# Kernel optimization log

Hardware: AMD Instinct MI355X
Metric: run time of the kernel (lower is better)

Reference implementation:

```python
import jax, jax.numpy as jnp
import numpy as np

THR = 0.2
BORDER_RM = 2
TEMPERATURE = 0.1


def _border_valid(hc, wc, b):
    # True for grid cells at least b away from every border; flattened to [hc*wc]
    ih = jnp.arange(hc)
    iw = jnp.arange(wc)
    vh = (ih >= b) & (ih < hc - b)
    vw = (iw >= b) & (iw < wc - b)
    return (vh[:, None] & vw[None, :]).reshape(-1)


def setup_inputs() -> dict:
    key = jax.random.key(0)
    k0, k1 = jax.random.split(key)
    N, C = 4, 256
    h0c = w0c = h1c = w1c = 64  # 512/8 coarse grid
    feat_c0 = jax.random.normal(k0, (N, h0c * w0c, C), dtype=jnp.float32)
    feat_c1 = jax.random.normal(k1, (N, h1c * w1c, C), dtype=jnp.float32)
    return {"feat_c0": feat_c0, "feat_c1": feat_c1,
            "h0c": h0c, "w0c": w0c, "h1c": h1c, "w1c": w1c}


def reference(feat_c0, feat_c1, h0c, w0c, h1c, w1c):
    C = feat_c0.shape[-1]
    inv_sqrt_c = 1.0 / np.sqrt(C)
    f0 = feat_c0 * inv_sqrt_c
    f1 = feat_c1 * inv_sqrt_c
    # [N, L, S] similarity, dual softmax
    sim = jnp.einsum('nlc,nsc->nls', f0, f1) / TEMPERATURE
    conf = jax.nn.softmax(sim, axis=1) * jax.nn.softmax(sim, axis=2)
    # threshold + border suppression (eval path: mask_border)
    mask = conf > THR
    v0 = _border_valid(h0c, w0c, BORDER_RM)  # [L]
    v1 = _border_valid(h1c, w1c, BORDER_RM)  # [S]
    mask = mask & v0[None, :, None] & v1[None, None, :]
    # mutual top-1 (argmax along both rows and columns)
    mask = mask & (conf == conf.max(axis=2, keepdims=True)) \
                & (conf == conf.max(axis=1, keepdims=True))
    # per-row match: padded fixed-shape form of torch.where(mask_v)
    mask_v = mask.any(axis=2)                     # [N, L] bool: row i has a match
    j_ids = jnp.argmax(mask, axis=2)              # [N, L] matched column (0 if none)
    mconf = jnp.take_along_axis(conf, j_ids[..., None], axis=2)[..., 0]
    mconf = jnp.where(mask_v, mconf, 0.0)         # zero where no match (== m_bids filter)
    return conf, mask_v, j_ids.astype(jnp.int32), mconf
```

## Files before the change

kernel.cpp:

```cpp
#include <hip/hip_runtime.h>

#define L_DIM 4096
#define C_DIM 256
#define NB 4

typedef __bf16 bf16x8 __attribute__((ext_vector_type(8)));
typedef float f32x4 __attribute__((ext_vector_type(4)));

#define GLB __attribute__((address_space(1)))
#define AS3 __attribute__((address_space(3)))

__global__ void init_ws(float* __restrict__ rsum, float* __restrict__ csum,
                        unsigned int* __restrict__ colmax,
                        unsigned long long* __restrict__ rowpack) {
    int i = blockIdx.x * 256 + threadIdx.x;
    if (i < NB * L_DIM) { rsum[i] = 0.f; csum[i] = 0.f; colmax[i] = 0u; rowpack[i] = 0ull; }
}

__global__ __launch_bounds__(256) void conv_k(const float* __restrict__ in,
                                              __bf16* __restrict__ out) {
    int i = blockIdx.x * 256 + threadIdx.x;
    const float4* p = (const float4*)in + (size_t)i * 2;
    float4 a = p[0], b = p[1];
    bf16x8 v;
    v[0]=(__bf16)a.x; v[1]=(__bf16)a.y; v[2]=(__bf16)a.z; v[3]=(__bf16)a.w;
    v[4]=(__bf16)b.x; v[5]=(__bf16)b.y; v[6]=(__bf16)b.z; v[7]=(__bf16)b.w;
    *(bf16x8*)&out[(size_t)i * 8] = v;
}

__global__ void recip_k(float* __restrict__ rsum, float* __restrict__ csum) {
    int i = blockIdx.x * 256 + threadIdx.x;
    if (i < NB * L_DIM) { rsum[i] = 1.0f / rsum[i]; csum[i] = 1.0f / csum[i]; }
}

template<bool PRE, int MODE>
__global__ __launch_bounds__(256) void gemm_pass(
        const float* __restrict__ f0, const float* __restrict__ f1,
        const __bf16* __restrict__ a_bf, const __bf16* __restrict__ b_bf,
        float* __restrict__ E,
        float* __restrict__ rsum, float* __restrict__ csum,
        unsigned long long* __restrict__ rowpack, unsigned int* __restrict__ colmax) {
    const int n  = blockIdx.z;
    const int tl = blockIdx.y;
    const int ts = blockIdx.x;

    constexpr int LDST = PRE ? 64 : 72;
    __shared__ __bf16 Al[128 * LDST];
    __shared__ __bf16 Bl[128 * LDST];

    const int t    = threadIdx.x;
    const int lane = t & 63;
    const int wave = t >> 6;
    const int wm   = wave >> 1, wn = wave & 1;
    const int q    = lane >> 4;
    const int l15  = lane & 15;

    const float* A = f0 + ((size_t)n * L_DIM + (size_t)tl * 128) * C_DIM;
    const float* B = f1 + ((size_t)n * L_DIM + (size_t)ts * 128) * C_DIM;
    const __bf16* gA = a_bf + ((size_t)n * L_DIM + (size_t)tl * 128) * C_DIM;
    const __bf16* gB = b_bf + ((size_t)n * L_DIM + (size_t)ts * 128) * C_DIM;

    f32x4 acc[4][4] = {};

    const int r8 = t >> 3;
    const int c8 = t & 7;
    const int lr = lane >> 3;
    const int lc = (lane & 7) * 8;

    for (int kt = 0; kt < C_DIM; kt += 64) {
        if constexpr (PRE) {
            #pragma unroll
            for (int i = 0; i < 4; ++i) {
                const int chunk = wave * 4 + i;
                const int row = chunk * 8 + lr;
                __builtin_amdgcn_global_load_lds(
                    (const GLB void*)(gA + (size_t)row * C_DIM + kt + lc),
                    (AS3 void*)&Al[chunk * 512], 16, 0, 0);
                __builtin_amdgcn_global_load_lds(
                    (const GLB void*)(gB + (size_t)row * C_DIM + kt + lc),
                    (AS3 void*)&Bl[chunk * 512], 16, 0, 0);
            }
        } else {
            #pragma unroll
            for (int i = 0; i < 4; ++i) {
                int row = r8 + 32 * i;
                const float4* pa = (const float4*)(A + (size_t)row * C_DIM + kt + c8 * 8);
                float4 a0 = pa[0], a1 = pa[1];
                const float4* pb = (const float4*)(B + (size_t)row * C_DIM + kt + c8 * 8);
                float4 b0 = pb[0], b1 = pb[1];
                bf16x8 av, bv;
                av[0]=(__bf16)a0.x; av[1]=(__bf16)a0.y; av[2]=(__bf16)a0.z; av[3]=(__bf16)a0.w;
                av[4]=(__bf16)a1.x; av[5]=(__bf16)a1.y; av[6]=(__bf16)a1.z; av[7]=(__bf16)a1.w;
                bv[0]=(__bf16)b0.x; bv[1]=(__bf16)b0.y; bv[2]=(__bf16)b0.z; bv[3]=(__bf16)b0.w;
                bv[4]=(__bf16)b1.x; bv[5]=(__bf16)b1.y; bv[6]=(__bf16)b1.z; bv[7]=(__bf16)b1.w;
                *(bf16x8*)&Al[row * LDST + c8 * 8] = av;
                *(bf16x8*)&Bl[row * LDST + c8 * 8] = bv;
            }
        }
        __syncthreads();
        #pragma unroll
        for (int k2 = 0; k2 < 2; ++k2) {
            const int kk = k2 * 32 + q * 8;
            bf16x8 af[4], bfv[4];
            #pragma unroll
            for (int mf = 0; mf < 4; ++mf)
                af[mf] = *(const bf16x8*)&Al[(wm * 64 + mf * 16 + l15) * LDST + kk];
            #pragma unroll
            for (int nf = 0; nf < 4; ++nf)
                bfv[nf] = *(const bf16x8*)&Bl[(wn * 64 + nf * 16 + l15) * LDST + kk];
            #pragma unroll
            for (int mf = 0; mf < 4; ++mf)
                #pragma unroll
                for (int nf = 0; nf < 4; ++nf)
                    acc[mf][nf] = __builtin_amdgcn_mfma_f32_16x16x32_bf16(
                        af[mf], bfv[nf], acc[mf][nf], 0, 0, 0);
        }
        __syncthreads();
    }

    const float scale = 0.0390625f;

    if constexpr (MODE == 0) {
        #pragma unroll
        for (int mf = 0; mf < 4; ++mf)
            #pragma unroll
            for (int nf = 0; nf < 4; ++nf)
                #pragma unroll
                for (int reg = 0; reg < 4; ++reg)
                    acc[mf][nf][reg] = __expf(acc[mf][nf][reg] * scale);

        {
            float rp[4][4];
            #pragma unroll
            for (int mf = 0; mf < 4; ++mf)
                #pragma unroll
                for (int reg = 0; reg < 4; ++reg) {
                    float v = acc[mf][0][reg] + acc[mf][1][reg] + acc[mf][2][reg] + acc[mf][3][reg];
                    v += __shfl_xor(v, 1); v += __shfl_xor(v, 2);
                    v += __shfl_xor(v, 4); v += __shfl_xor(v, 8);
                    rp[mf][reg] = v;
                }
            if (l15 == 0) {
                #pragma unroll
                for (int mf = 0; mf < 4; ++mf)
                    #pragma unroll
                    for (int reg = 0; reg < 4; ++reg)
                        atomicAdd(&rsum[n * L_DIM + tl * 128 + wm * 64 + mf * 16 + q * 4 + reg],
                                  rp[mf][reg]);
            }
        }
        {
            float cp[4];
            #pragma unroll
            for (int nf = 0; nf < 4; ++nf) {
                float v = 0.f;
                #pragma unroll
                for (int mf = 0; mf < 4; ++mf)
                    #pragma unroll
                    for (int reg = 0; reg < 4; ++reg)
                        v += acc[mf][nf][reg];
                v += __shfl_xor(v, 16); v += __shfl_xor(v, 32);
                cp[nf] = v;
            }
            if (q == 0) {
                #pragma unroll
                for (int nf = 0; nf < 4; ++nf)
                    atomicAdd(&csum[n * L_DIM + ts * 128 + wn * 64 + nf * 16 + l15], cp[nf]);
            }
        }
    } else {
        float vr[4][4];
        #pragma unroll
        for (int mf = 0; mf < 4; ++mf)
            #pragma unroll
            for (int reg = 0; reg < 4; ++reg)
                vr[mf][reg] = rsum[n * L_DIM + tl * 128 + wm * 64 + mf * 16 + q * 4 + reg];
        float vc[4];
        #pragma unroll
        for (int nf = 0; nf < 4; ++nf)
            vc[nf] = csum[n * L_DIM + ts * 128 + wn * 64 + nf * 16 + l15];

        float* Eb = E + (size_t)n * L_DIM * L_DIM + (size_t)tl * 128 * L_DIM + (size_t)ts * 128;

        unsigned int colbest[4] = {0u, 0u, 0u, 0u};
        #pragma unroll
        for (int mf = 0; mf < 4; ++mf) {
            #pragma unroll
            for (int reg = 0; reg < 4; ++reg) {
                unsigned long long best = 0ull;
                #pragma unroll
                for (int nf = 0; nf < 4; ++nf) {
                    float e = __expf(acc[mf][nf][reg] * scale);
                    float cf = e * e * vr[mf][reg] * vc[nf];
                    acc[mf][nf][reg] = cf;
                    unsigned int cb = __float_as_uint(cf);
                    unsigned int col = (unsigned int)(ts * 128 + wn * 64 + nf * 16 + l15);
                    unsigned long long p = ((unsigned long long)cb << 32) | (unsigned int)(~col);
                    best = p > best ? p : best;
                    colbest[nf] = cb > colbest[nf] ? cb : colbest[nf];
                }
                #pragma unroll
                for (int m = 1; m < 16; m <<= 1) {
                    unsigned int hi = (unsigned int)(best >> 32), lo = (unsigned int)best;
                    hi = __shfl_xor(hi, m); lo = __shfl_xor(lo, m);
                    unsigned long long o = ((unsigned long long)hi << 32) | lo;
                    best = o > best ? o : best;
                }
                if (l15 == 0)
                    atomicMax(&rowpack[n * L_DIM + tl * 128 + wm * 64 + mf * 16 + q * 4 + reg],
                              best);
            }
        }
        #pragma unroll
        for (int nf = 0; nf < 4; ++nf) {
            unsigned int cb = colbest[nf];
            unsigned int o = __shfl_xor(cb, 16); cb = o > cb ? o : cb;
            o = __shfl_xor(cb, 32); cb = o > cb ? o : cb;
            if (q == 0)
                atomicMax(&colmax[n * L_DIM + ts * 128 + wn * 64 + nf * 16 + l15], cb);
        }
        #pragma unroll
        for (int mf = 0; mf < 4; ++mf) {
            #pragma unroll
            for (int nf = 0; nf < 4; ++nf) {
                int col = wn * 64 + nf * 16 + l15;
                #pragma unroll
                for (int reg = 0; reg < 4; ++reg) {
                    int row = wm * 64 + mf * 16 + q * 4 + reg;
                    Eb[(size_t)row * L_DIM + col] = acc[mf][nf][reg];
                }
            }
        }
    }
}

__global__ void final_k(const unsigned long long* __restrict__ rowpack,
                        const unsigned int* __restrict__ colmax,
                        float* __restrict__ mask_out, float* __restrict__ j_out,
                        float* __restrict__ mconf_out) {
    int i = blockIdx.x * 256 + threadIdx.x;
    if (i >= NB * L_DIM) return;
    int n = i >> 12, l = i & 4095;
    unsigned long long rp = rowpack[i];
    float v = __uint_as_float((unsigned int)(rp >> 32));
    int s = (int)(~(unsigned int)(rp & 0xFFFFFFFFull));
    float cv = __uint_as_float(colmax[n * L_DIM + s]);
    int lh = l >> 6, lw = l & 63;
    int sh = s >> 6, sw = s & 63;
    bool bl = (lh >= 2) && (lh < 62) && (lw >= 2) && (lw < 62);
    bool bs = (sh >= 2) && (sh < 62) && (sw >= 2) && (sw < 62);
    bool m = (v > 0.2f) && bl && bs && (v == cv);
    mask_out[i]  = m ? 1.0f : 0.0f;
    j_out[i]     = m ? (float)s : 0.0f;
    mconf_out[i] = m ? v : 0.0f;
}

extern "C" void kernel_launch(void* const* d_in, const int* in_sizes, int n_in,
                              void* d_out, int out_size, void* d_ws, size_t ws_size,
                              hipStream_t stream) {
    const float* f0 = (const float*)d_in[0];
    const float* f1 = (const float*)d_in[1];

    float* out_conf  = (float*)d_out;
    float* out_mask  = out_conf + (size_t)NB * L_DIM * L_DIM;
    float* out_j     = out_mask + NB * L_DIM;
    float* out_mconf = out_j + NB * L_DIM;

    float* rsum = (float*)d_ws;
    float* csum = rsum + NB * L_DIM;
    unsigned int* colmax = (unsigned int*)(csum + NB * L_DIM);
    unsigned long long* rowpack = (unsigned long long*)(colmax + NB * L_DIM);
    __bf16* abf = (__bf16*)(rowpack + NB * L_DIM);
    __bf16* bbf = abf + (size_t)NB * L_DIM * C_DIM;

    size_t need = (size_t)(NB * L_DIM) * 20
                + 2 * (size_t)NB * L_DIM * C_DIM * sizeof(__bf16);
    bool pre = ws_size >= need;

    init_ws<<<dim3(64), dim3(256), 0, stream>>>(rsum, csum, colmax, rowpack);
    if (pre) {
        conv_k<<<dim3(2048), dim3(256), 0, stream>>>(f0, abf);
        conv_k<<<dim3(2048), dim3(256), 0, stream>>>(f1, bbf);
        gemm_pass<true, 0><<<dim3(32, 32, NB), dim3(256), 0, stream>>>(
            f0, f1, abf, bbf, nullptr, rsum, csum, nullptr, nullptr);
        recip_k<<<dim3(64), dim3(256), 0, stream>>>(rsum, csum);
        gemm_pass<true, 1><<<dim3(32, 32, NB), dim3(256), 0, stream>>>(
            f0, f1, abf, bbf, out_conf, rsum, csum, rowpack, colmax);
    } else {
        gemm_pass<false, 0><<<dim3(32, 32, NB), dim3(256), 0, stream>>>(
            f0, f1, nullptr, nullptr, nullptr, rsum, csum, nullptr, nullptr);
        recip_k<<<dim3(64), dim3(256), 0, stream>>>(rsum, csum);
        gemm_pass<false, 1><<<dim3(32, 32, NB), dim3(256), 0, stream>>>(
            f0, f1, nullptr, nullptr, out_conf, rsum, csum, rowpack, colmax);
    }
    final_k<<<dim3(64), dim3(256), 0, stream>>>(rowpack, colmax, out_mask, out_j, out_mconf);
}
```

Before: 495.9 us.

## Swizzle LDS loads, merge conversion kernels, fold reciprocal into epilogue, reorder stores

XOR-swizzles the column offset of the direct global-to-LDS bf16 loads and of the matching fragment reads, to cut LDS bank conflicts in the precomputed path. Merges the two bf16 conversion launches into one 2D grid and drops the reciprocal kernel by computing 1/rsum and 1/csum inline in the second pass. The second-pass exponent now uses a single exp with a doubled scale in place of squaring. The conf tile is stored before the row and column max reductions, and the column max is recomputed from the accumulators. Together these aim to remove launch overhead and shared-memory conflicts, at the cost of extra divisions per thread.

```diff
diff --git a/kernel.cpp b/kernel.cpp
--- a/kernel.cpp
+++ b/kernel.cpp
@@ -17,20 +17,19 @@
     if (i < NB * L_DIM) { rsum[i] = 0.f; csum[i] = 0.f; colmax[i] = 0u; rowpack[i] = 0ull; }
 }
 
-__global__ __launch_bounds__(256) void conv_k(const float* __restrict__ in,
-                                              __bf16* __restrict__ out) {
+__global__ __launch_bounds__(256) void conv_k(const float* __restrict__ f0,
+                                              const float* __restrict__ f1,
+                                              __bf16* __restrict__ abf,
+                                              __bf16* __restrict__ bbf) {
     int i = blockIdx.x * 256 + threadIdx.x;
+    const float* in = blockIdx.y ? f1 : f0;
+    __bf16* out = blockIdx.y ? bbf : abf;
     const float4* p = (const float4*)in + (size_t)i * 2;
     float4 a = p[0], b = p[1];
     bf16x8 v;
     v[0]=(__bf16)a.x; v[1]=(__bf16)a.y; v[2]=(__bf16)a.z; v[3]=(__bf16)a.w;
     v[4]=(__bf16)b.x; v[5]=(__bf16)b.y; v[6]=(__bf16)b.z; v[7]=(__bf16)b.w;
     *(bf16x8*)&out[(size_t)i * 8] = v;
-}
-
-__global__ void recip_k(float* __restrict__ rsum, float* __restrict__ csum) {
-    int i = blockIdx.x * 256 + threadIdx.x;
-    if (i < NB * L_DIM) { rsum[i] = 1.0f / rsum[i]; csum[i] = 1.0f / csum[i]; }
 }
 
 template<bool PRE, int MODE>
@@ -65,7 +64,7 @@
     const int r8 = t >> 3;
     const int c8 = t & 7;
     const int lr = lane >> 3;
-    const int lc = (lane & 7) * 8;
+    const int lc = ((lane & 7) ^ lr) * 8;
 
     for (int kt = 0; kt < C_DIM; kt += 64) {
         if constexpr (PRE) {
@@ -100,14 +99,16 @@
         __syncthreads();
         #pragma unroll
         for (int k2 = 0; k2 < 2; ++k2) {
-            const int kk = k2 * 32 + q * 8;
+            int off;
+            if constexpr (PRE) off = ((k2 * 4 + q) ^ (l15 & 7)) * 8;
+            else               off = k2 * 32 + q * 8;
             bf16x8 af[4], bfv[4];
             #pragma unroll
             for (int mf = 0; mf < 4; ++mf)
-                af[mf] = *(const bf16x8*)&Al[(wm * 64 + mf * 16 + l15) * LDST + kk];
+                af[mf] = *(const bf16x8*)&Al[(wm * 64 + mf * 16 + l15) * LDST + off];
             #pragma unroll
             for (int nf = 0; nf < 4; ++nf)
-                bfv[nf] = *(const bf16x8*)&Bl[(wn * 64 + nf * 16 + l15) * LDST + kk];
+                bfv[nf] = *(const bf16x8*)&Bl[(wn * 64 + nf * 16 + l15) * LDST + off];
             #pragma unroll
             for (int mf = 0; mf < 4; ++mf)
                 #pragma unroll
@@ -118,9 +119,8 @@
         __syncthreads();
     }
 
-    const float scale = 0.0390625f;
-
     if constexpr (MODE == 0) {
+        const float scale = 0.0390625f;
         #pragma unroll
         for (int mf = 0; mf < 4; ++mf)
             #pragma unroll
@@ -169,20 +169,41 @@
             }
         }
     } else {
+        const float scale2 = 0.078125f;
         float vr[4][4];
         #pragma unroll
         for (int mf = 0; mf < 4; ++mf)
             #pragma unroll
             for (int reg = 0; reg < 4; ++reg)
-                vr[mf][reg] = rsum[n * L_DIM + tl * 128 + wm * 64 + mf * 16 + q * 4 + reg];
+                vr[mf][reg] = 1.0f / rsum[n * L_DIM + tl * 128 + wm * 64 + mf * 16 + q * 4 + reg];
         float vc[4];
         #pragma unroll
         for (int nf = 0; nf < 4; ++nf)
-            vc[nf] = csum[n * L_DIM + ts * 128 + wn * 64 + nf * 16 + l15];
+            vc[nf] = 1.0f / csum[n * L_DIM + ts * 128 + wn * 64 + nf * 16 + l15];
+
+        #pragma unroll
+        for (int mf = 0; mf < 4; ++mf)
+            #pragma unroll
+            for (int nf = 0; nf < 4; ++nf)
+                #pragma unroll
+                for (int reg = 0; reg < 4; ++reg)
+                    acc[mf][nf][reg] =
+                        __expf(acc[mf][nf][reg] * scale2) * vr[mf][reg] * vc[nf];
 
         float* Eb = E + (size_t)n * L_DIM * L_DIM + (size_t)tl * 128 * L_DIM + (size_t)ts * 128;
-
-        unsigned int colbest[4] = {0u, 0u, 0u, 0u};
+        #pragma unroll
+        for (int mf = 0; mf < 4; ++mf) {
+            #pragma unroll
+            for (int nf = 0; nf < 4; ++nf) {
+                int col = wn * 64 + nf * 16 + l15;
+                #pragma unroll
+                for (int reg = 0; reg < 4; ++reg) {
+                    int row = wm * 64 + mf * 16 + q * 4 + reg;
+                    Eb[(size_t)row * L_DIM + col] = acc[mf][nf][reg];
+                }
+            }
+        }
+
         #pragma unroll
         for (int mf = 0; mf < 4; ++mf) {
             #pragma unroll
@@ -190,14 +211,10 @@
                 unsigned long long best = 0ull;
                 #pragma unroll
                 for (int nf = 0; nf < 4; ++nf) {
-                    float e = __expf(acc[mf][nf][reg] * scale);
-                    float cf = e * e * vr[mf][reg] * vc[nf];
-                    acc[mf][nf][reg] = cf;
-                    unsigned int cb = __float_as_uint(cf);
+                    unsigned int cb = __float_as_uint(acc[mf][nf][reg]);
                     unsigned int col = (unsigned int)(ts * 128 + wn * 64 + nf * 16 + l15);
                     unsigned long long p = ((unsigned long long)cb << 32) | (unsigned int)(~col);
                     best = p > best ? p : best;
-                    colbest[nf] = cb > colbest[nf] ? cb : colbest[nf];
                 }
                 #pragma unroll
                 for (int m = 1; m < 16; m <<= 1) {
@@ -213,23 +230,17 @@
         }
         #pragma unroll
         for (int nf = 0; nf < 4; ++nf) {
-            unsigned int cb = colbest[nf];
+            float m0 = acc[0][nf][0];
+            #pragma unroll
+            for (int mf = 0; mf < 4; ++mf)
+                #pragma unroll
+                for (int reg = 0; reg < 4; ++reg)
+                    m0 = fmaxf(m0, acc[mf][nf][reg]);
+            unsigned int cb = __float_as_uint(m0);
             unsigned int o = __shfl_xor(cb, 16); cb = o > cb ? o : cb;
             o = __shfl_xor(cb, 32); cb = o > cb ? o : cb;
             if (q == 0)
                 atomicMax(&colmax[n * L_DIM + ts * 128 + wn * 64 + nf * 16 + l15], cb);
-        }
-        #pragma unroll
-        for (int mf = 0; mf < 4; ++mf) {
-            #pragma unroll
-            for (int nf = 0; nf < 4; ++nf) {
-                int col = wn * 64 + nf * 16 + l15;
-                #pragma unroll
-                for (int reg = 0; reg < 4; ++reg) {
-                    int row = wm * 64 + mf * 16 + q * 4 + reg;
-                    Eb[(size_t)row * L_DIM + col] = acc[mf][nf][reg];
-                }
-            }
         }
     }
 }
@@ -279,17 +290,14 @@
 
     init_ws<<<dim3(64), dim3(256), 0, stream>>>(rsum, csum, colmax, rowpack);
     if (pre) {
-        conv_k<<<dim3(2048), dim3(256), 0, stream>>>(f0, abf);
-        conv_k<<<dim3(2048), dim3(256), 0, stream>>>(f1, bbf);
+        conv_k<<<dim3(2048, 2), dim3(256), 0, stream>>>(f0, f1, abf, bbf);
         gemm_pass<true, 0><<<dim3(32, 32, NB), dim3(256), 0, stream>>>(
             f0, f1, abf, bbf, nullptr, rsum, csum, nullptr, nullptr);
-        recip_k<<<dim3(64), dim3(256), 0, stream>>>(rsum, csum);
         gemm_pass<true, 1><<<dim3(32, 32, NB), dim3(256), 0, stream>>>(
             f0, f1, abf, bbf, out_conf, rsum, csum, rowpack, colmax);
     } else {
         gemm_pass<false, 0><<<dim3(32, 32, NB), dim3(256), 0, stream>>>(
             f0, f1, nullptr, nullptr, nullptr, rsum, csum, nullptr, nullptr);
-        recip_k<<<dim3(64), dim3(256), 0, stream>>>(rsum, csum);
         gemm_pass<false, 1><<<dim3(32, 32, NB), dim3(256), 0, stream>>>(
             f0, f1, nullptr, nullptr, out_conf, rsum, csum, rowpack, colmax);
     }
```

Measured after the change: 455.8 us. -8.1%, faster.
